# Optimization experiments

Measured on AMD Instinct MI355X. Metric: run time of the kernel, lower is better.

## Reference

```python
import jax, jax.numpy as jnp
import numpy as np

N, C, T, V, O, S, R = 32, 64, 256, 25, 192, 3, 8  # batch, in_ch, time, joints, out_ch, subsets, rel_ch


def setup_inputs() -> dict:
    key = jax.random.key(0)
    ks = jax.random.split(key, 20)
    w = lambda i, shape: (jax.random.normal(ks[i], shape, jnp.float32) * 0.05)
    return {
        "x": jax.random.normal(ks[0], (N, C, T, V), jnp.float32),
        "spd_A": jax.random.normal(ks[1], (V, V), jnp.float32) * 0.1,
        "A3": jax.random.normal(ks[2], (S, V, V), jnp.float32) * 0.1,
        "A6": jax.random.normal(ks[3], (6, V, V), jnp.float32) * 0.1,
        "conv1_w": w(4, (S, R, C)), "conv1_b": jnp.zeros((S, R), jnp.float32),
        "conv2_w": w(5, (S, R, C)), "conv2_b": jnp.zeros((S, R), jnp.float32),
        "conv4_w": w(6, (S, O, R)), "conv4_b": jnp.zeros((S, O), jnp.float32),
        "conv3_w": w(7, (S, O, C)), "conv3_b": jnp.zeros((S, O), jnp.float32),
        "alpha": jnp.full((1,), 0.5, jnp.float32),
        "beta": jnp.full((1,), 0.5, jnp.float32),
        "gamma": jnp.full((1,), 0.5, jnp.float32),
        "bn_w": jnp.ones((O,), jnp.float32), "bn_b": jnp.zeros((O,), jnp.float32),
        "down_w": w(8, (O, C)), "down_b": jnp.zeros((O,), jnp.float32),
        "dbn_w": jnp.ones((O,), jnp.float32), "dbn_b": jnp.zeros((O,), jnp.float32),
    }


def _bn(y, w, b):
    # BatchNorm2d in training mode: stats over (N, T, V) per channel, biased var
    mu = y.mean(axis=(0, 2, 3), keepdims=True)
    var = ((y - mu) ** 2).mean(axis=(0, 2, 3), keepdims=True)
    return (y - mu) * jax.lax.rsqrt(var + 1e-5) * w[None, :, None, None] + b[None, :, None, None]


def reference(x, spd_A, A3, A6, conv1_w, conv1_b, conv2_w, conv2_b, conv4_w, conv4_b,
              conv3_w, conv3_b, alpha, beta, gamma, bn_w, bn_b, down_w, down_b, dbn_w, dbn_b):
    out_c = conv4_w.shape[1]
    # A6 expanded: (out//6, 6, V, V) -> (out, V, V); contiguous-view == tile along channel blocks
    A6_ex = jnp.tile(A6, (out_c // 6, 1, 1))  # (O, V, V)
    # 1x1 conv then temporal mean == conv on temporal mean (linear op commutes)
    xm = x.mean(axis=2)  # (N, C, V)
    x1 = jnp.einsum('ncv,src->nsrv', xm, conv1_w) + conv1_b[None, :, :, None]
    x2 = jnp.einsum('ncv,src->nsrv', xm, conv2_w) + conv2_b[None, :, :, None]
    d = jnp.tanh(x1[..., :, None] - x2[..., None, :])  # (N, S, R, V, V)
    A_dyn = jnp.einsum('nsruv,sor->nsouv', d, conv4_w) + conv4_b[None, :, :, None, None]
    A_at = (A_dyn * alpha + A3[None, :, None, :, :]
            + A6_ex[None, None] * beta + spd_A[None, None, None] * gamma)  # (N, S, O, V, V)
    # CTRGC_2: x3 = conv3(x); einsum 'ncuv,nctv->nctu', summed over subsets
    x3 = jnp.einsum('nctv,soc->nsotv', x, conv3_w) + conv3_b[None, :, :, None, None]
    y = jnp.einsum('nsouv,nsotv->notu', A_at, x3)  # (N, O, T, V)
    y = _bn(y, bn_w, bn_b)
    xd = jnp.einsum('nctv,oc->notv', x, down_w) + down_b[None, :, None, None]
    y = jax.nn.relu(y + _bn(xd, dbn_w, dbn_b))
    return y
```

## Files before the change

kernel.cpp:

```cpp
#include <hip/hip_runtime.h>

#define N_ 32
#define C_ 64
#define T_ 256
#define V_ 25
#define O_ 192
#define S_ 3
#define R_ 8
#define VV (V_*V_)
#define TV (T_*V_)
#define RP 26
#define TRP (T_*RP)

typedef unsigned short u16;
typedef unsigned int u32;
typedef __attribute__((ext_vector_type(4))) u16 u16x4;
typedef __attribute__((ext_vector_type(8))) u16 u16x8;
typedef __attribute__((ext_vector_type(4))) u32 u32x4;
typedef __attribute__((ext_vector_type(8))) __bf16 bf16x8;
typedef __attribute__((ext_vector_type(4))) float f32x4;

#define WS_A2F_U 0
#define WS_XQ_U  (18874368)
#define WS_XD_U  (18874368 + 13631488)
#define WS_XM_F   (35913728)
#define WS_RS_F   (35913728 + 51200)
#define WS_STAT_F (35913728 + 51200 + 153600)
#define WS_COEF_F (35913728 + 51200 + 153600 + 768)

__device__ __forceinline__ u16 f2b(float f) {
    return __builtin_bit_cast(u16, (__bf16)f);
}
__device__ __forceinline__ float b2f(u16 u) {
    return __builtin_bit_cast(float, ((unsigned)u) << 16);
}
__device__ __forceinline__ f32x4 mfma16(bf16x8 a, bf16x8 b, f32x4 c) {
    return __builtin_amdgcn_mfma_f32_16x16x32_bf16(a, b, c, 0, 0, 0);
}

__global__ void k0_xq(const float* __restrict__ x, u16* __restrict__ xq) {
    __shared__ float tile[64][52];
    int bid = blockIdx.x;
    int n = bid >> 7, tb = bid & 127;
    int t0 = tb * 2;
    int tid = threadIdx.x;
    const float2* xp = (const float2*)(x + (size_t)n * C_ * TV + t0 * 25);
    for (int p = tid; p < 1600; p += 256) {
        int c = p / 25, q = p % 25;
        float2 f2 = xp[(size_t)c * 3200 + q];
        tile[c][q * 2] = f2.x;
        tile[c][q * 2 + 1] = f2.y;
    }
    __syncthreads();
    for (int p = tid; p < 832; p += 256) {
        int row = p >> 4, c4g = p & 15;
        int t = row >= RP, v = row - t * RP;
        u16x4 w;
        #pragma unroll
        for (int i = 0; i < 4; ++i) {
            int co = ((c4g & 3) << 4) + ((c4g >> 2) << 2) + i;
            w[i] = (v < 25) ? f2b(tile[co][t * 25 + v]) : (u16)0;
        }
        *(u16x4*)&xq[((size_t)n * TRP + tb * 52 + row) * 64 + c4g * 4] = w;
    }
}

__global__ void k1_xm(const float* __restrict__ x, float* __restrict__ xm_out) {
    __shared__ float ps[256];
    int nc = blockIdx.x;
    int tid = threadIdx.x;
    const float* xp = x + (size_t)nc * TV;
    float acc = 0.f;
    if (tid < 250) {
        int tg = tid / 25, v = tid % 25;
        for (int j = 0; j < 26; ++j) {
            int t = tg + 10 * j;
            if (t < T_) acc += xp[t * V_ + v];
        }
    }
    ps[tid] = acc;
    __syncthreads();
    if (tid < V_) {
        float s = 0.f;
        for (int tg = 0; tg < 10; ++tg) s += ps[tg * 25 + tid];
        xm_out[(size_t)nc * V_ + tid] = s * (1.f / T_);
    }
}

__global__ void k2_a2f(const float* __restrict__ spd, const float* __restrict__ A3,
                       const float* __restrict__ A6,
                       const float* __restrict__ w1, const float* __restrict__ b1,
                       const float* __restrict__ w2, const float* __restrict__ b2,
                       const float* __restrict__ w4, const float* __restrict__ b4,
                       const float* __restrict__ b3,
                       const float* __restrict__ alpha, const float* __restrict__ beta,
                       const float* __restrict__ gamma,
                       u16* __restrict__ a2f, const float* __restrict__ xmbuf,
                       float* __restrict__ rs_tot) {
    __shared__ float xm[C_ * V_];
    __shared__ float x1s[R_ * V_], x2s[R_ * V_];
    __shared__ float dm[R_ * VV];
    __shared__ float a3s[VV], sps[VV], a6s[6 * VV];
    __shared__ float aat[2 * VV];
    __shared__ float w4s[2][R_];
    __shared__ float b4s[2];
    int bid = blockIdx.x;
    int n = bid / 24;
    int rem = bid % 24;
    int s = rem / 8, og = rem % 8;
    int tid = threadIdx.x;
    const float* xmg = xmbuf + (size_t)n * C_ * V_;
    for (int p = tid; p < C_ * V_; p += 256) xm[p] = xmg[p];
    for (int p = tid; p < VV; p += 256) { a3s[p] = A3[s * VV + p]; sps[p] = spd[p]; }
    for (int p = tid; p < 6 * VV; p += 256) a6s[p] = A6[p];
    __syncthreads();
    if (tid < R_ * V_) {
        int r = tid / V_, v = tid % V_;
        float acc1 = b1[s * R_ + r], acc2 = b2[s * R_ + r];
        for (int c = 0; c < C_; ++c) {
            float xv = xm[c * V_ + v];
            acc1 += xv * w1[(s * R_ + r) * C_ + c];
            acc2 += xv * w2[(s * R_ + r) * C_ + c];
        }
        x1s[tid] = acc1; x2s[tid] = acc2;
    }
    __syncthreads();
    for (int p = tid; p < R_ * VV; p += 256) {
        int r = p / VV, uv = p % VV, u = uv / V_, v = uv % V_;
        dm[p] = tanhf(x1s[r * V_ + u] - x2s[r * V_ + v]);
    }
    __syncthreads();
    float al = alpha[0], be = beta[0], ga = gamma[0];
    for (int op = 0; op < 12; ++op) {
        int o0 = og * 24 + op * 2;
        if (tid < 16) w4s[tid >> 3][tid & 7] =
            w4[((size_t)(s * O_ + o0 + (tid >> 3))) * R_ + (tid & 7)];
        if (tid < 2) b4s[tid] = b4[s * O_ + o0 + tid];
        __syncthreads();
        for (int p = tid; p < 2 * VV; p += 256) {
            int oo = p / VV, pp = p % VV;
            float acc = b4s[oo];
            #pragma unroll
            for (int r = 0; r < R_; ++r) acc += dm[r * VV + pp] * w4s[oo][r];
            int o = o0 + oo;
            aat[p] = al * acc + a3s[pp] + be * a6s[(o % 6) * VV + pp] + ga * sps[pp];
        }
        __syncthreads();
        if (tid < 2 * V_) {
            int oo = tid / V_, u = tid % V_;
            float rs = 0.f;
            for (int v = 0; v < V_; ++v) rs += aat[oo * VV + u * V_ + v];
            atomicAdd(&rs_tot[((size_t)(n * O_ + o0 + oo)) * V_ + u],
                      b3[s * O_ + o0 + oo] * rs);
        }
        {
            int oo = tid >> 7, l2 = tid & 127, cu = l2 >> 6, l = l2 & 63;
            int u = cu * 16 + (l & 15);
            u16x8 w;
            #pragma unroll
            for (int j = 0; j < 8; ++j) {
                int v = ((j >> 2) << 4) + ((l >> 4) << 2) + (j & 3);
                float val = 0.f;
                if (u < V_ && v < V_) val = aat[oo * VV + u * V_ + v];
                w[j] = f2b(val);
            }
            size_t idx = ((((size_t)(n * O_ + o0 + oo)) * S_ + s) * 2 + cu) * 64 + l;
            ((u16x8*)a2f)[idx] = w;
        }
        __syncthreads();
    }
}

#define OSTR_B 2504
#define SSTR_B 832
#define BUF_B  20096

__global__ __launch_bounds__(256, 3)
void k3_main(const u16* __restrict__ xq,
             const float* __restrict__ w3, const float* __restrict__ dw,
             const float* __restrict__ db,
             const u16* __restrict__ a2f, const float* __restrict__ rs_tot,
             float* __restrict__ yout, u16* __restrict__ xdws,
             float* __restrict__ stats) {
    __shared__ char x3Lb[2 * BUF_B];
    int orig = blockIdx.x;
    int bid = (orig & 7) * 96 + (orig >> 3);
    int n = bid / 24;
    int o0 = (bid % 24) * 8;
    int tid = threadIdx.x, wid = tid >> 6, lane = tid & 63;
    int lr = lane & 15, lg = lane >> 4;
    int colt = wid & 1;
    int rt0 = (wid >> 1) * 13;

    for (int p = tid; p < 2 * BUF_B / 16; p += 256) ((u32x4*)x3Lb)[p] = u32x4{0,0,0,0};

    const float* wsrc = (colt == 0)
        ? w3 + ((size_t)((lr >> 3) * O_ + o0 + (lr & 7))) * C_
        : ((lr < 8) ? w3 + ((size_t)(2 * O_ + o0 + lr)) * C_
                    : dw + ((size_t)(o0 + lr - 8)) * C_);
    bf16x8 bw[2];
    #pragma unroll
    for (int ks = 0; ks < 2; ++ks) {
        u16x8 tmp;
        #pragma unroll
        for (int j = 0; j < 8; ++j) {
            int c = ks * 32 + (lg << 2) + (j & 3) + ((j >> 2) << 4);
            tmp[j] = f2b(wsrc[c]);
        }
        bw[ks] = __builtin_bit_cast(bf16x8, tmp);
    }
    float dbv = (colt == 1 && lr >= 8) ? db[o0 + lr - 8] : 0.f;

    int wo = (colt == 0) ? (lr & 7) : lr;
    int wsb = (colt == 0) ? (lr >> 3) : 2;
    int colbyte = wo * OSTR_B + wsb * SSTR_B;

    const bf16x8* a2v = (const bf16x8*)a2f;
    bf16x8 Bh[2][6];
    float rsb0[2], rsb1[2];
    #pragma unroll
    for (int oi = 0; oi < 2; ++oi) {
        int o = o0 + (wid << 1) + oi;
        const bf16x8* bp = a2v + ((size_t)(n * O_ + o)) * 6 * 64 + lane;
        #pragma unroll
        for (int q = 0; q < 6; ++q) Bh[oi][q] = bp[(size_t)q * 64];
        const float* rsp = rs_tot + ((size_t)(n * O_ + o)) * V_;
        rsb0[oi] = rsp[lr];
        rsb1[oi] = (lr < 9) ? rsp[16 + lr] : 0.f;
    }

    float sy1[2] = {0, 0}, sy2[2] = {0, 0};
    float sd1 = 0.f, sd2 = 0.f;
    const u16* xbn = xq + (size_t)n * TRP * 64;
    int rdw = 13 * lr + 2 * lg;
    __syncthreads();

    for (int ch = 0; ch < 16; ++ch) {
        int t0 = ch * 16;
        char* buf = x3Lb + (ch & 1) * BUF_B;
        const u16* xrow = xbn + (size_t)t0 * RP * 64;
        for (int rt = rt0; rt < rt0 + 13; ++rt) {
            const u16* ap = xrow + (size_t)(rt * 16 + lr) * 64 + (lg << 4);
            u16x8 A0 = *(const u16x8*)ap;
            u16x8 A1 = *(const u16x8*)(ap + 8);
            f32x4 acc = {0.f, 0.f, 0.f, 0.f};
            acc = mfma16(__builtin_bit_cast(bf16x8, A0), bw[0], acc);
            acc = mfma16(__builtin_bit_cast(bf16x8, A1), bw[1], acc);
            int rbase = rt * 16 + (lg << 2);
            if (colt == 0 || lr < 8) {
                u16x4 w;
                #pragma unroll
                for (int reg = 0; reg < 4; ++reg) w[reg] = f2b(acc[reg]);
                *(u16x4*)(buf + colbyte + rbase * 2) = w;
            } else {
                size_t xdb = ((size_t)(n * O_ + o0 + lr - 8)) * TV + (size_t)t0 * V_;
                #pragma unroll
                for (int reg = 0; reg < 4; ++reg) {
                    int rr = rbase + reg;
                    int t = rr / RP, v = rr - t * RP;
                    if (v < 25) {
                        float val = acc[reg] + dbv;
                        xdws[xdb + t * V_ + v] = f2b(val);
                        sd1 += val; sd2 += val * val;
                    }
                }
            }
        }
        __syncthreads();
        #pragma unroll
        for (int oi = 0; oi < 2; ++oi) {
            int ol = (wid << 1) + oi;
            int o = o0 + ol;
            const u32* L = (const u32*)(buf + ol * OSTR_B);
            f32x4 acc0 = {0, 0, 0, 0}, acc1 = {0, 0, 0, 0};
            #pragma unroll
            for (int s = 0; s < 3; ++s) {
                const u32* Ls = L + s * 208 + rdw;
                u32 d0 = Ls[0], d1 = Ls[1], d8 = Ls[8], d9 = Ls[9];
                bf16x8 A = __builtin_bit_cast(bf16x8, u32x4{d0, d1, d8, d9});
                acc0 = mfma16(A, Bh[oi][s * 2 + 0], acc0);
                acc1 = mfma16(A, Bh[oi][s * 2 + 1], acc1);
            }
            size_t yb = ((size_t)(n * O_ + o) * T_ + t0 + (lg << 2)) * V_;
            #pragma unroll
            for (int reg = 0; reg < 4; ++reg) {
                float v0 = acc0[reg] + rsb0[oi];
                yout[yb + (size_t)reg * V_ + lr] = v0;
                sy1[oi] += v0; sy2[oi] += v0 * v0;
                if (lr < 9) {
                    float v1 = acc1[reg] + rsb1[oi];
                    yout[yb + (size_t)reg * V_ + 16 + lr] = v1;
                    sy1[oi] += v1; sy2[oi] += v1 * v1;
                }
            }
        }
    }
    #pragma unroll
    for (int oi = 0; oi < 2; ++oi) {
        float v1 = sy1[oi], v2 = sy2[oi];
        #pragma unroll
        for (int m = 1; m < 64; m <<= 1) {
            v1 += __shfl_xor(v1, m);
            v2 += __shfl_xor(v2, m);
        }
        if (lane == 0) {
            atomicAdd(&stats[0 * O_ + o0 + (wid << 1) + oi], v1);
            atomicAdd(&stats[1 * O_ + o0 + (wid << 1) + oi], v2);
        }
    }
    if (colt == 1) {
        float v1 = sd1, v2 = sd2;
        v1 += __shfl_xor(v1, 16); v2 += __shfl_xor(v2, 16);
        v1 += __shfl_xor(v1, 32); v2 += __shfl_xor(v2, 32);
        if (lane >= 8 && lane < 16) {
            atomicAdd(&stats[2 * O_ + o0 + lane - 8], v1);
            atomicAdd(&stats[3 * O_ + o0 + lane - 8], v2);
        }
    }
}

__global__ void k4_coef(const float* __restrict__ bn_w, const float* __restrict__ bn_b,
                        const float* __restrict__ dbn_w, const float* __restrict__ dbn_b,
                        const float* __restrict__ stats, float* __restrict__ coef) {
    int o = threadIdx.x;
    if (o >= O_) return;
    float inv = 1.f / (float)(N_ * T_ * V_);
    float mu_y = stats[o] * inv;
    float var_y = stats[O_ + o] * inv - mu_y * mu_y;
    float ay = bn_w[o] * rsqrtf(var_y + 1e-5f);
    float by = bn_b[o] - mu_y * ay;
    float mu_d = stats[2 * O_ + o] * inv;
    float var_d = stats[3 * O_ + o] * inv - mu_d * mu_d;
    float ad = dbn_w[o] * rsqrtf(var_d + 1e-5f);
    float bd = dbn_b[o] - mu_d * ad;
    coef[o] = ay; coef[O_ + o] = by; coef[2 * O_ + o] = ad; coef[3 * O_ + o] = bd;
}

__global__ void k5_final(float* __restrict__ out, const u16* __restrict__ xd,
                         const float* __restrict__ cf) {
    size_t total = (size_t)N_ * O_ * TV / 8;
    for (size_t i = blockIdx.x * (size_t)blockDim.x + threadIdx.x; i < total;
         i += (size_t)gridDim.x * blockDim.x) {
        int o = (int)((i / 800) % O_);
        float ay = cf[o], by = cf[O_ + o], ad = cf[2 * O_ + o], bd = cf[3 * O_ + o];
        float4 y0 = ((float4*)out)[2 * i];
        float4 y1 = ((float4*)out)[2 * i + 1];
        u16x8 dv = ((const u16x8*)xd)[i];
        float4 r0, r1;
        r0.x = fmaxf(ay * y0.x + by + ad * b2f(dv[0]) + bd, 0.f);
        r0.y = fmaxf(ay * y0.y + by + ad * b2f(dv[1]) + bd, 0.f);
        r0.z = fmaxf(ay * y0.z + by + ad * b2f(dv[2]) + bd, 0.f);
        r0.w = fmaxf(ay * y0.w + by + ad * b2f(dv[3]) + bd, 0.f);
        r1.x = fmaxf(ay * y1.x + by + ad * b2f(dv[4]) + bd, 0.f);
        r1.y = fmaxf(ay * y1.y + by + ad * b2f(dv[5]) + bd, 0.f);
        r1.z = fmaxf(ay * y1.z + by + ad * b2f(dv[6]) + bd, 0.f);
        r1.w = fmaxf(ay * y1.w + by + ad * b2f(dv[7]) + bd, 0.f);
        ((float4*)out)[2 * i] = r0;
        ((float4*)out)[2 * i + 1] = r1;
    }
}

extern "C" void kernel_launch(void* const* d_in, const int* in_sizes, int n_in,
                              void* d_out, int out_size, void* d_ws, size_t ws_size,
                              hipStream_t stream) {
    const float* x     = (const float*)d_in[0];
    const float* spd   = (const float*)d_in[1];
    const float* A3    = (const float*)d_in[2];
    const float* A6    = (const float*)d_in[3];
    const float* w1    = (const float*)d_in[4];
    const float* b1    = (const float*)d_in[5];
    const float* w2    = (const float*)d_in[6];
    const float* b2    = (const float*)d_in[7];
    const float* w4    = (const float*)d_in[8];
    const float* b4    = (const float*)d_in[9];
    const float* w3    = (const float*)d_in[10];
    const float* b3    = (const float*)d_in[11];
    const float* alpha = (const float*)d_in[12];
    const float* beta  = (const float*)d_in[13];
    const float* gamma = (const float*)d_in[14];
    const float* bn_w  = (const float*)d_in[15];
    const float* bn_b  = (const float*)d_in[16];
    const float* dw    = (const float*)d_in[17];
    const float* db    = (const float*)d_in[18];
    const float* dbn_w = (const float*)d_in[19];
    const float* dbn_b = (const float*)d_in[20];
    float* out = (float*)d_out;
    u16*   wsu = (u16*)d_ws;
    float* wsf = (float*)d_ws;

    u16* a2f  = wsu + WS_A2F_U;
    u16* xq   = wsu + WS_XQ_U;
    u16* xd   = wsu + WS_XD_U;
    float* xm    = wsf + WS_XM_F;
    float* rs    = wsf + WS_RS_F;
    float* stats = wsf + WS_STAT_F;
    float* coef  = wsf + WS_COEF_F;

    hipMemsetAsync(rs, 0, (N_ * O_ * V_ + 4 * O_) * sizeof(float), stream);

    k0_xq<<<N_ * 128, 256, 0, stream>>>(x, xq);
    k1_xm<<<N_ * C_, 256, 0, stream>>>(x, xm);
    k2_a2f<<<N_ * S_ * 8, 256, 0, stream>>>(spd, A3, A6, w1, b1, w2, b2, w4, b4, b3,
                                            alpha, beta, gamma, a2f, xm, rs);
    k3_main<<<N_ * 24, 256, 0, stream>>>(xq, w3, dw, db, a2f, rs, out, xd, stats);
    k4_coef<<<1, 256, 0, stream>>>(bn_w, bn_b, dbn_w, dbn_b, stats, coef);
    k5_final<<<4096, 256, 0, stream>>>(out, xd, coef);
}
```

Measured before the change: 366.3 us.

## Make k3_main waves independent: per-wave LDS staging, split time across blocks, prefetch

Each wave now owns four output channels and its own LDS slice. It computes the x3 conv and the downsample columns for those channels, then consumes them itself, so the block-wide __syncthreads between the conv and aggregation phases goes away. Blocks now cover 16 channels and half of the time range instead of 8 channels over the full range. The next A tile is prefetched from global memory inside the row loop. The trade-off is that each wave recomputes the full conv over all rows for its channels, holds more registers (Bh now has 4x6 entries), and needs a larger LDS footprint.

```diff
diff --git a/kernel.cpp b/kernel.cpp
--- a/kernel.cpp
+++ b/kernel.cpp
@@ -171,9 +171,8 @@
     }
 }
 
-#define OSTR_B 2504
-#define SSTR_B 832
-#define BUF_B  20096
+#define CSTR_B 840
+#define WAVE_B (12*CSTR_B)
 
 __global__ __launch_bounds__(256, 3)
 void k3_main(const u16* __restrict__ xq,
@@ -182,22 +181,25 @@
              const u16* __restrict__ a2f, const float* __restrict__ rs_tot,
              float* __restrict__ yout, u16* __restrict__ xdws,
              float* __restrict__ stats) {
-    __shared__ char x3Lb[2 * BUF_B];
+    __shared__ u32x4 x3q[(4 * WAVE_B + 64) / 16];
+    char* x3Lb = (char*)x3q;
     int orig = blockIdx.x;
     int bid = (orig & 7) * 96 + (orig >> 3);
     int n = bid / 24;
-    int o0 = (bid % 24) * 8;
+    int rem = bid % 24;
+    int o0b = (rem >> 1) * 16;
+    int th = rem & 1;
     int tid = threadIdx.x, wid = tid >> 6, lane = tid & 63;
     int lr = lane & 15, lg = lane >> 4;
-    int colt = wid & 1;
-    int rt0 = (wid >> 1) * 13;
-
-    for (int p = tid; p < 2 * BUF_B / 16; p += 256) ((u32x4*)x3Lb)[p] = u32x4{0,0,0,0};
-
-    const float* wsrc = (colt == 0)
-        ? w3 + ((size_t)((lr >> 3) * O_ + o0 + (lr & 7))) * C_
-        : ((lr < 8) ? w3 + ((size_t)(2 * O_ + o0 + lr)) * C_
-                    : dw + ((size_t)(o0 + lr - 8)) * C_);
+    int o0w = o0b + wid * 4;
+    char* wbase = x3Lb + wid * WAVE_B;
+
+    for (int p = lane; p < (WAVE_B + 64) / 16; p += 64)
+        ((u32x4*)wbase)[p] = u32x4{0, 0, 0, 0};
+
+    const float* wsrc = (lr < 12)
+        ? w3 + ((size_t)((lr >> 2) * O_ + o0w + (lr & 3))) * C_
+        : dw + ((size_t)(o0w + (lr & 3))) * C_;
     bf16x8 bw[2];
     #pragma unroll
     for (int ks = 0; ks < 2; ++ks) {
@@ -209,18 +211,14 @@
         }
         bw[ks] = __builtin_bit_cast(bf16x8, tmp);
     }
-    float dbv = (colt == 1 && lr >= 8) ? db[o0 + lr - 8] : 0.f;
-
-    int wo = (colt == 0) ? (lr & 7) : lr;
-    int wsb = (colt == 0) ? (lr >> 3) : 2;
-    int colbyte = wo * OSTR_B + wsb * SSTR_B;
+    float dbv = (lr >= 12) ? db[o0w + (lr & 3)] : 0.f;
 
     const bf16x8* a2v = (const bf16x8*)a2f;
-    bf16x8 Bh[2][6];
-    float rsb0[2], rsb1[2];
+    bf16x8 Bh[4][6];
+    float rsb0[4], rsb1[4];
     #pragma unroll
-    for (int oi = 0; oi < 2; ++oi) {
-        int o = o0 + (wid << 1) + oi;
+    for (int oi = 0; oi < 4; ++oi) {
+        int o = o0w + oi;
         const bf16x8* bp = a2v + ((size_t)(n * O_ + o)) * 6 * 64 + lane;
         #pragma unroll
         for (int q = 0; q < 6; ++q) Bh[oi][q] = bp[(size_t)q * 64];
@@ -229,31 +227,35 @@
         rsb1[oi] = (lr < 9) ? rsp[16 + lr] : 0.f;
     }
 
-    float sy1[2] = {0, 0}, sy2[2] = {0, 0};
+    float sy1[4] = {0, 0, 0, 0}, sy2[4] = {0, 0, 0, 0};
     float sd1 = 0.f, sd2 = 0.f;
     const u16* xbn = xq + (size_t)n * TRP * 64;
-    int rdw = 13 * lr + 2 * lg;
-    __syncthreads();
-
-    for (int ch = 0; ch < 16; ++ch) {
-        int t0 = ch * 16;
-        char* buf = x3Lb + (ch & 1) * BUF_B;
-        const u16* xrow = xbn + (size_t)t0 * RP * 64;
-        for (int rt = rt0; rt < rt0 + 13; ++rt) {
-            const u16* ap = xrow + (size_t)(rt * 16 + lr) * 64 + (lg << 4);
-            u16x8 A0 = *(const u16x8*)ap;
-            u16x8 A1 = *(const u16x8*)(ap + 8);
+    char* wcol = wbase + lr * CSTR_B + lg * 8;
+    const char* rbl = wbase + 52 * lr + 8 * lg;
+
+    for (int ch = 0; ch < 8; ++ch) {
+        int t0 = th * 128 + ch * 16;
+        const u16* app = xbn + (size_t)t0 * RP * 64 + (size_t)lr * 64 + (lg << 4);
+        u16x8 A0 = *(const u16x8*)app;
+        u16x8 A1 = *(const u16x8*)(app + 8);
+        for (int rt = 0; rt < 26; ++rt) {
+            u16x8 nA0 = A0, nA1 = A1;
+            if (rt < 25) {
+                const u16* np = app + (rt + 1) * 1024;
+                nA0 = *(const u16x8*)np;
+                nA1 = *(const u16x8*)(np + 8);
+            }
             f32x4 acc = {0.f, 0.f, 0.f, 0.f};
             acc = mfma16(__builtin_bit_cast(bf16x8, A0), bw[0], acc);
             acc = mfma16(__builtin_bit_cast(bf16x8, A1), bw[1], acc);
-            int rbase = rt * 16 + (lg << 2);
-            if (colt == 0 || lr < 8) {
+            if (lr < 12) {
                 u16x4 w;
                 #pragma unroll
                 for (int reg = 0; reg < 4; ++reg) w[reg] = f2b(acc[reg]);
-                *(u16x4*)(buf + colbyte + rbase * 2) = w;
+                *(u16x4*)(wcol + rt * 32) = w;
             } else {
-                size_t xdb = ((size_t)(n * O_ + o0 + lr - 8)) * TV + (size_t)t0 * V_;
+                int rbase = rt * 16 + (lg << 2);
+                size_t xdb = ((size_t)(n * O_ + o0w + (lr & 3))) * TV + (size_t)t0 * V_;
                 #pragma unroll
                 for (int reg = 0; reg < 4; ++reg) {
                     int rr = rbase + reg;
@@ -265,18 +267,19 @@
                     }
                 }
             }
-        }
-        __syncthreads();
+            A0 = nA0; A1 = nA1;
+        }
         #pragma unroll
-        for (int oi = 0; oi < 2; ++oi) {
-            int ol = (wid << 1) + oi;
-            int o = o0 + ol;
-            const u32* L = (const u32*)(buf + ol * OSTR_B);
+        for (int oi = 0; oi < 4; ++oi) {
+            int o = o0w + oi;
             f32x4 acc0 = {0, 0, 0, 0}, acc1 = {0, 0, 0, 0};
             #pragma unroll
             for (int s = 0; s < 3; ++s) {
-                const u32* Ls = L + s * 208 + rdw;
-                u32 d0 = Ls[0], d1 = Ls[1], d8 = Ls[8], d9 = Ls[9];
+                const char* p = rbl + (s * 4 + oi) * CSTR_B;
+                u32 d0 = *(const u32*)(p);
+                u32 d1 = *(const u32*)(p + 4);
+                u32 d8 = *(const u32*)(p + 32);
+                u32 d9 = *(const u32*)(p + 36);
                 bf16x8 A = __builtin_bit_cast(bf16x8, u32x4{d0, d1, d8, d9});
                 acc0 = mfma16(A, Bh[oi][s * 2 + 0], acc0);
                 acc1 = mfma16(A, Bh[oi][s * 2 + 1], acc1);
@@ -296,7 +299,7 @@
         }
     }
     #pragma unroll
-    for (int oi = 0; oi < 2; ++oi) {
+    for (int oi = 0; oi < 4; ++oi) {
         float v1 = sy1[oi], v2 = sy2[oi];
         #pragma unroll
         for (int m = 1; m < 64; m <<= 1) {
@@ -304,17 +307,17 @@
             v2 += __shfl_xor(v2, m);
         }
         if (lane == 0) {
-            atomicAdd(&stats[0 * O_ + o0 + (wid << 1) + oi], v1);
-            atomicAdd(&stats[1 * O_ + o0 + (wid << 1) + oi], v2);
-        }
-    }
-    if (colt == 1) {
+            atomicAdd(&stats[0 * O_ + o0w + oi], v1);
+            atomicAdd(&stats[1 * O_ + o0w + oi], v2);
+        }
+    }
+    {
         float v1 = sd1, v2 = sd2;
         v1 += __shfl_xor(v1, 16); v2 += __shfl_xor(v2, 16);
         v1 += __shfl_xor(v1, 32); v2 += __shfl_xor(v2, 32);
-        if (lane >= 8 && lane < 16) {
-            atomicAdd(&stats[2 * O_ + o0 + lane - 8], v1);
-            atomicAdd(&stats[3 * O_ + o0 + lane - 8], v2);
+        if (lane >= 12 && lane < 16) {
+            atomicAdd(&stats[2 * O_ + o0w + lane - 12], v1);
+            atomicAdd(&stats[3 * O_ + o0w + lane - 12], v2);
         }
     }
 }
```

New measurement: 407.2 us. 1.11x slower.

## Split adjacency kernel per output pair and prefetch x tiles in main kernel

Applied to the files above, without the earlier changes.

The adjacency-building kernel now launches one block per (batch, subset, output-channel pair) instead of looping 12 times per block. It recomputes tanh differences inline instead of staging them in shared memory, which raises parallelism and removes the per-iteration barriers. The main kernel adds a 6-deep register prefetch pipeline for the bf16 x tiles across the unrolled row-tile loop, to hide global load latency behind MFMAs. The costs are redundant recompute of the x1/x2 projections and tanh in every block, plus higher register pressure, and the prefetch reads past the last chunk.

```diff
diff --git a/kernel.cpp b/kernel.cpp
--- a/kernel.cpp
+++ b/kernel.cpp
@@ -99,20 +99,26 @@
                        float* __restrict__ rs_tot) {
     __shared__ float xm[C_ * V_];
     __shared__ float x1s[R_ * V_], x2s[R_ * V_];
-    __shared__ float dm[R_ * VV];
-    __shared__ float a3s[VV], sps[VV], a6s[6 * VV];
+    __shared__ float a3s[VV], sps[VV];
+    __shared__ float a6p[2 * VV];
     __shared__ float aat[2 * VV];
     __shared__ float w4s[2][R_];
     __shared__ float b4s[2];
     int bid = blockIdx.x;
-    int n = bid / 24;
-    int rem = bid % 24;
-    int s = rem / 8, og = rem % 8;
+    int n = bid / (S_ * 96);
+    int r2 = bid % (S_ * 96);
+    int s = r2 / 96, o0 = (r2 % 96) * 2;
     int tid = threadIdx.x;
     const float* xmg = xmbuf + (size_t)n * C_ * V_;
     for (int p = tid; p < C_ * V_; p += 256) xm[p] = xmg[p];
     for (int p = tid; p < VV; p += 256) { a3s[p] = A3[s * VV + p]; sps[p] = spd[p]; }
-    for (int p = tid; p < 6 * VV; p += 256) a6s[p] = A6[p];
+    {
+        int e0 = o0 % 6;
+        for (int p = tid; p < 2 * VV; p += 256) a6p[p] = A6[e0 * VV + p];
+    }
+    if (tid < 16) w4s[tid >> 3][tid & 7] =
+        w4[((size_t)(s * O_ + o0 + (tid >> 3))) * R_ + (tid & 7)];
+    if (tid < 2) b4s[tid] = b4[s * O_ + o0 + tid];
     __syncthreads();
     if (tid < R_ * V_) {
         int r = tid / V_, v = tid % V_;
@@ -125,49 +131,41 @@
         x1s[tid] = acc1; x2s[tid] = acc2;
     }
     __syncthreads();
-    for (int p = tid; p < R_ * VV; p += 256) {
-        int r = p / VV, uv = p % VV, u = uv / V_, v = uv % V_;
-        dm[p] = tanhf(x1s[r * V_ + u] - x2s[r * V_ + v]);
-    }
-    __syncthreads();
     float al = alpha[0], be = beta[0], ga = gamma[0];
-    for (int op = 0; op < 12; ++op) {
-        int o0 = og * 24 + op * 2;
-        if (tid < 16) w4s[tid >> 3][tid & 7] =
-            w4[((size_t)(s * O_ + o0 + (tid >> 3))) * R_ + (tid & 7)];
-        if (tid < 2) b4s[tid] = b4[s * O_ + o0 + tid];
-        __syncthreads();
-        for (int p = tid; p < 2 * VV; p += 256) {
-            int oo = p / VV, pp = p % VV;
-            float acc = b4s[oo];
-            #pragma unroll
-            for (int r = 0; r < R_; ++r) acc += dm[r * VV + pp] * w4s[oo][r];
-            int o = o0 + oo;
-            aat[p] = al * acc + a3s[pp] + be * a6s[(o % 6) * VV + pp] + ga * sps[pp];
-        }
-        __syncthreads();
-        if (tid < 2 * V_) {
-            int oo = tid / V_, u = tid % V_;
-            float rs = 0.f;
-            for (int v = 0; v < V_; ++v) rs += aat[oo * VV + u * V_ + v];
-            atomicAdd(&rs_tot[((size_t)(n * O_ + o0 + oo)) * V_ + u],
-                      b3[s * O_ + o0 + oo] * rs);
-        }
-        {
-            int oo = tid >> 7, l2 = tid & 127, cu = l2 >> 6, l = l2 & 63;
-            int u = cu * 16 + (l & 15);
-            u16x8 w;
-            #pragma unroll
-            for (int j = 0; j < 8; ++j) {
-                int v = ((j >> 2) << 4) + ((l >> 4) << 2) + (j & 3);
-                float val = 0.f;
-                if (u < V_ && v < V_) val = aat[oo * VV + u * V_ + v];
-                w[j] = f2b(val);
-            }
-            size_t idx = ((((size_t)(n * O_ + o0 + oo)) * S_ + s) * 2 + cu) * 64 + l;
-            ((u16x8*)a2f)[idx] = w;
-        }
-        __syncthreads();
+    for (int p = tid; p < VV; p += 256) {
+        int u = p / V_, v = p % V_;
+        float acc0 = b4s[0], acc1 = b4s[1];
+        #pragma unroll
+        for (int r = 0; r < R_; ++r) {
+            float d = tanhf(x1s[r * V_ + u] - x2s[r * V_ + v]);
+            acc0 += d * w4s[0][r];
+            acc1 += d * w4s[1][r];
+        }
+        float base = a3s[p] + ga * sps[p];
+        aat[p]      = al * acc0 + base + be * a6p[p];
+        aat[VV + p] = al * acc1 + base + be * a6p[VV + p];
+    }
+    __syncthreads();
+    if (tid < 2 * V_) {
+        int oo = tid / V_, u = tid % V_;
+        float rs = 0.f;
+        for (int v = 0; v < V_; ++v) rs += aat[oo * VV + u * V_ + v];
+        atomicAdd(&rs_tot[((size_t)(n * O_ + o0 + oo)) * V_ + u],
+                  b3[s * O_ + o0 + oo] * rs);
+    }
+    {
+        int oo = tid >> 7, l2 = tid & 127, cu = l2 >> 6, l = l2 & 63;
+        int u = cu * 16 + (l & 15);
+        u16x8 w;
+        #pragma unroll
+        for (int j = 0; j < 8; ++j) {
+            int v = ((j >> 2) << 4) + ((l >> 4) << 2) + (j & 3);
+            float val = 0.f;
+            if (u < V_ && v < V_) val = aat[oo * VV + u * V_ + v];
+            w[j] = f2b(val);
+        }
+        size_t idx = ((((size_t)(n * O_ + o0 + oo)) * S_ + s) * 2 + cu) * 64 + l;
+        ((u16x8*)a2f)[idx] = w;
     }
 }
 
@@ -232,21 +230,34 @@
     float sy1[2] = {0, 0}, sy2[2] = {0, 0};
     float sd1 = 0.f, sd2 = 0.f;
     const u16* xbn = xq + (size_t)n * TRP * 64;
+    const u16* lanep = xbn + (size_t)(rt0 * 16 + lr) * 64 + (lg << 4);
     int rdw = 13 * lr + 2 * lg;
     __syncthreads();
 
+    u16x8 a0, a1, a2, a3, a4, a5, b0, b1, b2, b3, b4, b5;
+    a0 = *(const u16x8*)(lanep + 0 * 1024); b0 = *(const u16x8*)(lanep + 0 * 1024 + 8);
+    a1 = *(const u16x8*)(lanep + 1 * 1024); b1 = *(const u16x8*)(lanep + 1 * 1024 + 8);
+    a2 = *(const u16x8*)(lanep + 2 * 1024); b2 = *(const u16x8*)(lanep + 2 * 1024 + 8);
+    a3 = *(const u16x8*)(lanep + 3 * 1024); b3 = *(const u16x8*)(lanep + 3 * 1024 + 8);
+    a4 = *(const u16x8*)(lanep + 4 * 1024); b4 = *(const u16x8*)(lanep + 4 * 1024 + 8);
+    a5 = *(const u16x8*)(lanep + 5 * 1024); b5 = *(const u16x8*)(lanep + 5 * 1024 + 8);
+
     for (int ch = 0; ch < 16; ++ch) {
+        char* buf = x3Lb + (ch & 1) * BUF_B;
+        const u16* cbase = lanep + ch * 26624;
         int t0 = ch * 16;
-        char* buf = x3Lb + (ch & 1) * BUF_B;
-        const u16* xrow = xbn + (size_t)t0 * RP * 64;
-        for (int rt = rt0; rt < rt0 + 13; ++rt) {
-            const u16* ap = xrow + (size_t)(rt * 16 + lr) * 64 + (lg << 4);
-            u16x8 A0 = *(const u16x8*)ap;
-            u16x8 A1 = *(const u16x8*)(ap + 8);
+        #pragma unroll
+        for (int i = 0; i < 13; ++i) {
             f32x4 acc = {0.f, 0.f, 0.f, 0.f};
-            acc = mfma16(__builtin_bit_cast(bf16x8, A0), bw[0], acc);
-            acc = mfma16(__builtin_bit_cast(bf16x8, A1), bw[1], acc);
-            int rbase = rt * 16 + (lg << 2);
+            acc = mfma16(__builtin_bit_cast(bf16x8, a0), bw[0], acc);
+            acc = mfma16(__builtin_bit_cast(bf16x8, b0), bw[1], acc);
+            a0 = a1; b0 = b1; a1 = a2; b1 = b2; a2 = a3; b2 = b3;
+            a3 = a4; b3 = b4; a4 = a5; b4 = b5;
+            const u16* np = (i < 7) ? (cbase + (i + 6) * 1024)
+                                    : (cbase + 26624 + (i - 7) * 1024);
+            a5 = *(const u16x8*)np;
+            b5 = *(const u16x8*)(np + 8);
+            int rbase = (rt0 + i) * 16 + (lg << 2);
             if (colt == 0 || lr < 8) {
                 u16x4 w;
                 #pragma unroll
@@ -400,8 +411,8 @@
 
     k0_xq<<<N_ * 128, 256, 0, stream>>>(x, xq);
     k1_xm<<<N_ * C_, 256, 0, stream>>>(x, xm);
-    k2_a2f<<<N_ * S_ * 8, 256, 0, stream>>>(spd, A3, A6, w1, b1, w2, b2, w4, b4, b3,
-                                            alpha, beta, gamma, a2f, xm, rs);
+    k2_a2f<<<N_ * S_ * 96, 256, 0, stream>>>(spd, A3, A6, w1, b1, w2, b2, w4, b4, b3,
+                                             alpha, beta, gamma, a2f, xm, rs);
     k3_main<<<N_ * 24, 256, 0, stream>>>(xq, w3, dw, db, a2f, rs, out, xd, stats);
     k4_coef<<<1, 256, 0, stream>>>(bn_w, bn_b, dbn_w, dbn_b, stats, coef);
     k5_final<<<4096, 256, 0, stream>>>(out, xd, coef);
```

Measured after the change: 510.2 us. 39.3% more time.

## Process 32-timestep chunks per warp with both weight column tiles, single LDS buffer

Applied to the files above, without the earlier changes.

Each warp now computes both column tiles (two MFMA pairs sharing the same A fragment) for 13 row tiles of a 32-timestep chunk, rather than one column tile over half the rows of a 16-timestep chunk. The x tile loaded from global is reused across twice as many output columns and the chunk loop runs 8 iterations instead of 16. The double-buffered LDS is replaced by one larger buffer, which adds a second barrier per chunk. The intent is to halve the global x reads and loop overhead, at the cost of more registers and the extra synchronisation.

```diff
diff --git a/kernel.cpp b/kernel.cpp
--- a/kernel.cpp
+++ b/kernel.cpp
@@ -171,9 +171,9 @@
     }
 }
 
-#define OSTR_B 2504
-#define SSTR_B 832
-#define BUF_B  20096
+#define SSTR_B 1664
+#define OSTR_B (3*SSTR_B + 20)
+#define BUF_B  (8*OSTR_B + 64)
 
 __global__ __launch_bounds__(256, 3)
 void k3_main(const u16* __restrict__ xq,
@@ -182,38 +182,37 @@
              const u16* __restrict__ a2f, const float* __restrict__ rs_tot,
              float* __restrict__ yout, u16* __restrict__ xdws,
              float* __restrict__ stats) {
-    __shared__ char x3Lb[2 * BUF_B];
+    __shared__ char x3Lb[BUF_B];
     int orig = blockIdx.x;
     int bid = (orig & 7) * 96 + (orig >> 3);
     int n = bid / 24;
     int o0 = (bid % 24) * 8;
     int tid = threadIdx.x, wid = tid >> 6, lane = tid & 63;
     int lr = lane & 15, lg = lane >> 4;
-    int colt = wid & 1;
-    int rt0 = (wid >> 1) * 13;
-
-    for (int p = tid; p < 2 * BUF_B / 16; p += 256) ((u32x4*)x3Lb)[p] = u32x4{0,0,0,0};
-
-    const float* wsrc = (colt == 0)
-        ? w3 + ((size_t)((lr >> 3) * O_ + o0 + (lr & 7))) * C_
-        : ((lr < 8) ? w3 + ((size_t)(2 * O_ + o0 + lr)) * C_
-                    : dw + ((size_t)(o0 + lr - 8)) * C_);
-    bf16x8 bw[2];
+
+    for (int p = tid; p < BUF_B / 16; p += 256) ((u32x4*)x3Lb)[p] = u32x4{0, 0, 0, 0};
+
+    const float* wA = (lr < 8) ? w3 + ((size_t)(0 * O_ + o0 + lr)) * C_
+                               : w3 + ((size_t)(1 * O_ + o0 + lr - 8)) * C_;
+    const float* wB = (lr < 8) ? w3 + ((size_t)(2 * O_ + o0 + lr)) * C_
+                               : dw + ((size_t)(o0 + lr - 8)) * C_;
+    bf16x8 bwA[2], bwB[2];
     #pragma unroll
     for (int ks = 0; ks < 2; ++ks) {
-        u16x8 tmp;
+        u16x8 ta, tb;
         #pragma unroll
         for (int j = 0; j < 8; ++j) {
             int c = ks * 32 + (lg << 2) + (j & 3) + ((j >> 2) << 4);
-            tmp[j] = f2b(wsrc[c]);
-        }
-        bw[ks] = __builtin_bit_cast(bf16x8, tmp);
-    }
-    float dbv = (colt == 1 && lr >= 8) ? db[o0 + lr - 8] : 0.f;
-
-    int wo = (colt == 0) ? (lr & 7) : lr;
-    int wsb = (colt == 0) ? (lr >> 3) : 2;
-    int colbyte = wo * OSTR_B + wsb * SSTR_B;
+            ta[j] = f2b(wA[c]);
+            tb[j] = f2b(wB[c]);
+        }
+        bwA[ks] = __builtin_bit_cast(bf16x8, ta);
+        bwB[ks] = __builtin_bit_cast(bf16x8, tb);
+    }
+    float dbv = (lr >= 8) ? db[o0 + lr - 8] : 0.f;
+
+    int colbyteA = ((lr < 8) ? lr * OSTR_B : (lr - 8) * OSTR_B + SSTR_B) + (lg << 3);
+    int colbyteB = lr * OSTR_B + 2 * SSTR_B + (lg << 3);
 
     const bf16x8* a2v = (const bf16x8*)a2f;
     bf16x8 Bh[2][6];
@@ -235,32 +234,40 @@
     int rdw = 13 * lr + 2 * lg;
     __syncthreads();
 
-    for (int ch = 0; ch < 16; ++ch) {
-        int t0 = ch * 16;
-        char* buf = x3Lb + (ch & 1) * BUF_B;
-        const u16* xrow = xbn + (size_t)t0 * RP * 64;
-        for (int rt = rt0; rt < rt0 + 13; ++rt) {
-            const u16* ap = xrow + (size_t)(rt * 16 + lr) * 64 + (lg << 4);
+    for (int ch = 0; ch < 8; ++ch) {
+        const u16* xrow = xbn + (size_t)(ch * 832) * 64;
+        for (int i = 0; i < 13; ++i) {
+            int tile = wid * 13 + i;
+            const u16* ap = xrow + (size_t)(tile * 16 + lr) * 64 + (lg << 4);
             u16x8 A0 = *(const u16x8*)ap;
             u16x8 A1 = *(const u16x8*)(ap + 8);
-            f32x4 acc = {0.f, 0.f, 0.f, 0.f};
-            acc = mfma16(__builtin_bit_cast(bf16x8, A0), bw[0], acc);
-            acc = mfma16(__builtin_bit_cast(bf16x8, A1), bw[1], acc);
-            int rbase = rt * 16 + (lg << 2);
-            if (colt == 0 || lr < 8) {
-                u16x4 w;
+            f32x4 accA = {0.f, 0.f, 0.f, 0.f};
+            f32x4 accB = {0.f, 0.f, 0.f, 0.f};
+            accA = mfma16(__builtin_bit_cast(bf16x8, A0), bwA[0], accA);
+            accA = mfma16(__builtin_bit_cast(bf16x8, A1), bwA[1], accA);
+            accB = mfma16(__builtin_bit_cast(bf16x8, A0), bwB[0], accB);
+            accB = mfma16(__builtin_bit_cast(bf16x8, A1), bwB[1], accB);
+            int rbase = tile * 16 + (lg << 2);
+            {
+                u16x4 wa;
                 #pragma unroll
-                for (int reg = 0; reg < 4; ++reg) w[reg] = f2b(acc[reg]);
-                *(u16x4*)(buf + colbyte + rbase * 2) = w;
+                for (int reg = 0; reg < 4; ++reg) wa[reg] = f2b(accA[reg]);
+                *(u16x4*)(x3Lb + colbyteA + rbase * 2 - (lg << 3)) = wa;
+            }
+            if (lr < 8) {
+                u16x4 wb;
+                #pragma unroll
+                for (int reg = 0; reg < 4; ++reg) wb[reg] = f2b(accB[reg]);
+                *(u16x4*)(x3Lb + colbyteB + rbase * 2 - (lg << 3)) = wb;
             } else {
-                size_t xdb = ((size_t)(n * O_ + o0 + lr - 8)) * TV + (size_t)t0 * V_;
+                size_t xdb = ((size_t)(n * O_ + o0 + lr - 8)) * TV;
                 #pragma unroll
                 for (int reg = 0; reg < 4; ++reg) {
                     int rr = rbase + reg;
-                    int t = rr / RP, v = rr - t * RP;
+                    int tl = rr / RP, v = rr - tl * RP;
                     if (v < 25) {
-                        float val = acc[reg] + dbv;
-                        xdws[xdb + t * V_ + v] = f2b(val);
+                        float val = accB[reg] + dbv;
+                        xdws[xdb + (ch * 32 + tl) * V_ + v] = f2b(val);
                         sd1 += val; sd2 += val * val;
                     }
                 }
@@ -268,32 +275,36 @@
         }
         __syncthreads();
         #pragma unroll
-        for (int oi = 0; oi < 2; ++oi) {
-            int ol = (wid << 1) + oi;
-            int o = o0 + ol;
-            const u32* L = (const u32*)(buf + ol * OSTR_B);
-            f32x4 acc0 = {0, 0, 0, 0}, acc1 = {0, 0, 0, 0};
+        for (int j = 0; j < 2; ++j) {
             #pragma unroll
-            for (int s = 0; s < 3; ++s) {
-                const u32* Ls = L + s * 208 + rdw;
-                u32 d0 = Ls[0], d1 = Ls[1], d8 = Ls[8], d9 = Ls[9];
-                bf16x8 A = __builtin_bit_cast(bf16x8, u32x4{d0, d1, d8, d9});
-                acc0 = mfma16(A, Bh[oi][s * 2 + 0], acc0);
-                acc1 = mfma16(A, Bh[oi][s * 2 + 1], acc1);
-            }
-            size_t yb = ((size_t)(n * O_ + o) * T_ + t0 + (lg << 2)) * V_;
-            #pragma unroll
-            for (int reg = 0; reg < 4; ++reg) {
-                float v0 = acc0[reg] + rsb0[oi];
-                yout[yb + (size_t)reg * V_ + lr] = v0;
-                sy1[oi] += v0; sy2[oi] += v0 * v0;
-                if (lr < 9) {
-                    float v1 = acc1[reg] + rsb1[oi];
-                    yout[yb + (size_t)reg * V_ + 16 + lr] = v1;
-                    sy1[oi] += v1; sy2[oi] += v1 * v1;
+            for (int oi = 0; oi < 2; ++oi) {
+                int ol = (wid << 1) + oi;
+                int o = o0 + ol;
+                const u32* L = (const u32*)(x3Lb + ol * OSTR_B) + j * 208 + rdw;
+                f32x4 acc0 = {0, 0, 0, 0}, acc1 = {0, 0, 0, 0};
+                #pragma unroll
+                for (int s = 0; s < 3; ++s) {
+                    const u32* Ls = L + s * 416;
+                    u32 d0 = Ls[0], d1 = Ls[1], d8 = Ls[8], d9 = Ls[9];
+                    bf16x8 A = __builtin_bit_cast(bf16x8, u32x4{d0, d1, d8, d9});
+                    acc0 = mfma16(A, Bh[oi][s * 2 + 0], acc0);
+                    acc1 = mfma16(A, Bh[oi][s * 2 + 1], acc1);
+                }
+                size_t yb = ((size_t)(n * O_ + o) * T_ + ch * 32 + j * 16 + (lg << 2)) * V_;
+                #pragma unroll
+                for (int reg = 0; reg < 4; ++reg) {
+                    float v0 = acc0[reg] + rsb0[oi];
+                    yout[yb + (size_t)reg * V_ + lr] = v0;
+                    sy1[oi] += v0; sy2[oi] += v0 * v0;
+                    if (lr < 9) {
+                        float v1 = acc1[reg] + rsb1[oi];
+                        yout[yb + (size_t)reg * V_ + 16 + lr] = v1;
+                        sy1[oi] += v1; sy2[oi] += v1 * v1;
+                    }
                 }
             }
         }
+        __syncthreads();
     }
     #pragma unroll
     for (int oi = 0; oi < 2; ++oi) {
@@ -308,7 +319,7 @@
             atomicAdd(&stats[1 * O_ + o0 + (wid << 1) + oi], v2);
         }
     }
-    if (colt == 1) {
+    {
         float v1 = sd1, v2 = sd2;
         v1 += __shfl_xor(v1, 16); v2 += __shfl_xor(v2, 16);
         v1 += __shfl_xor(v1, 32); v2 += __shfl_xor(v2, 32);
```

Result: no change. 370.7 us (+1.2%).
